# Kernel tuning notes

Measured on AMD Instinct MI355X. Metric: run time of the kernel, lower is better.

Reference implementation:

```python
import math
import jax, jax.numpy as jnp
import numpy as np

B, T, C, H = 4, 2048, 1024, 1024

def setup_inputs() -> dict:
    key = jax.random.key(0)
    kx, kk, kq, kv = jax.random.split(key, 4)
    s = 1.0 / math.sqrt(C)
    return {
        "x": jax.random.normal(kx, (B, T, C), dtype=jnp.float32),
        # torch Linear weight is [out, in]; store transposed [in, out] for x @ W
        "Wk": jax.random.uniform(kk, (C, H), dtype=jnp.float32, minval=-s, maxval=s),
        "Wq": jax.random.uniform(kq, (C, H), dtype=jnp.float32, minval=-s, maxval=s),
        "Wv": jax.random.uniform(kv, (C, H), dtype=jnp.float32, minval=-s, maxval=s),
    }

def reference(x, Wk, Wq, Wv):
    K = x @ Wk  # [B,T,H]
    Q = x @ Wq
    V = x @ Wv
    scale = 1.0 / math.sqrt(K.shape[-1])
    wei = jnp.einsum('bth,bsh->bts', Q, K) * scale  # [B,T,T]
    t = x.shape[1]
    causal = jnp.tril(jnp.ones((t, t), dtype=bool))
    wei = jnp.where(causal, wei, -jnp.inf)
    wei = jax.nn.softmax(wei, axis=-1)
    wei = jax.nn.relu(wei)  # no-op mathematically but kept for fidelity
    return jnp.einsum('bts,bsh->bth', wei, V)
```

## Files before the change

### kernel.cpp

```cpp
#include <hip/hip_runtime.h>

typedef _Float16 f16;
typedef _Float16 f16x8 __attribute__((ext_vector_type(8)));
typedef float    f32x4 __attribute__((ext_vector_type(4)));

#define AS3 __attribute__((address_space(3)))
#define AS1 __attribute__((address_space(1)))

static __device__ __forceinline__ void gld_lds16(const f16* g, f16* l) {
    __builtin_amdgcn_global_load_lds((const AS1 void*)g, (AS3 void*)l, 16, 0, 0);
}

static __device__ __forceinline__ unsigned pack_f16(float a, float b) {
    union { f16 h[2]; unsigned u; } p;
    p.h[0] = (f16)a; p.h[1] = (f16)b;
    return p.u;
}

__global__ void cvt_fused(const float* __restrict__ x, f16* __restrict__ xh,
                          const float* __restrict__ Wq, const float* __restrict__ Wk,
                          const float* __restrict__ Wv, f16* __restrict__ Wt) {
    __shared__ float tile[32][33];
    const int bid = blockIdx.x;
    if (bid < 4096) {
        int i = bid * 256 + threadIdx.x;
        const f32x4* xv = (const f32x4*)x;
        f32x4 a = xv[2 * i], b = xv[2 * i + 1];
        f16x8 h;
        h[0] = (f16)a[0]; h[1] = (f16)a[1]; h[2] = (f16)a[2]; h[3] = (f16)a[3];
        h[4] = (f16)b[0]; h[5] = (f16)b[1]; h[6] = (f16)b[2]; h[7] = (f16)b[3];
        ((f16x8*)xh)[i] = h;
    } else {
        int b2 = bid - 4096;
        int bx = b2 & 31, by = (b2 >> 5) & 31, bz = b2 >> 10;
        const float* W = bz == 0 ? Wq : (bz == 1 ? Wk : Wv);
        int tx = threadIdx.x & 31, ty = threadIdx.x >> 5;
        int n0 = bx * 32, k0 = by * 32;
#pragma unroll
        for (int r = 0; r < 4; ++r)
            tile[ty + r * 8][tx] = W[(size_t)(k0 + ty + r * 8) * 1024 + n0 + tx];
        __syncthreads();
        f16* o = Wt + (size_t)bz * 1024 * 1024;
#pragma unroll
        for (int r = 0; r < 4; ++r)
            o[(size_t)(n0 + ty + r * 8) * 1024 + k0 + tx] = (f16)tile[tx][ty + r * 8];
    }
}

template <int MODE>
__global__ __launch_bounds__(256, 4)
void gemm128(const f16* __restrict__ A, int lda, long aStride,
             const f16* __restrict__ B, int ldb, long bStride,
             void* __restrict__ Cout, int ldc, long cStride,
             int ktiles, float scale,
             const f16* __restrict__ A2, const f16* __restrict__ B2,
             void* __restrict__ C2) {
    int bm, bn, bz = blockIdx.z;
    int m0, n0;
    const f16 *Ab, *Bb;
    char* Cb;

    if (MODE == 0) {
        bn = blockIdx.x; bm = blockIdx.y;
        n0 = bn * 128;
        if (bm < 64) {
            m0 = bm * 128;
            Ab = A; Bb = B; Cb = (char*)Cout;
        } else {
            int t = bm - 64;
            int bb = t >> 3;
            m0 = (t & 7) * 128;
            Ab = A2;
            Bb = B2 + (long)bb * 2048 * 1024;
            Cb = (char*)C2 + (long)bb * 1024 * 2048 * sizeof(f16);
        }
    } else if (MODE == 1) {
        int i = blockIdx.x;
        float ff = sqrtf(8.f * (float)i + 1.f);
        bm = (int)((ff - 1.f) * 0.5f);
        while ((bm + 1) * (bm + 2) / 2 <= i) ++bm;
        while (bm * (bm + 1) / 2 > i) --bm;
        bn = i - bm * (bm + 1) / 2;
        m0 = bm * 128; n0 = bn * 128;
        Ab = A + (long)bz * aStride;
        Bb = B + (long)bz * bStride;
        Cb = (char*)Cout + (long)bz * cStride * sizeof(f16);
    } else {
        bn = blockIdx.x; bm = gridDim.y - 1 - blockIdx.y;
        int lim = 4 * (bm + 1); if (lim < ktiles) ktiles = lim;
        m0 = bm * 128; n0 = bn * 128;
        Ab = A + (long)bz * aStride;
        Bb = B + (long)bz * bStride;
        Cb = (char*)Cout + (long)bz * cStride * sizeof(float);
    }

    __shared__ f16 lds[2 * 8192];

    const int tid = threadIdx.x;
    const int wave = tid >> 6, lane = tid & 63;
    const int q = lane >> 4, rr = lane & 15;
    const int wm = (wave >> 1) * 64, wn = (wave & 1) * 64;

    const int kcs = (((tid & 3) - (lane >> 4)) & 3) * 8;
    const f16* pA = Ab + (long)(m0 + (tid >> 2)) * lda + kcs;
    const f16* pB = Bb + (long)(n0 + (tid >> 2)) * ldb + kcs;

    auto stage = [&](int kt, int buf) {
        const int k0 = kt * 32;
        f16* lA = lds + buf * 8192 + wave * 512;
        f16* lB = lds + buf * 8192 + 4096 + wave * 512;
#pragma unroll
        for (int it = 0; it < 2; ++it) {
            gld_lds16(pA + (long)it * 64 * lda + k0, lA + it * 2048);
            gld_lds16(pB + (long)it * 64 * ldb + k0, lB + it * 2048);
        }
    };

    const int slotf = ((q + (rr >> 2)) & 3) * 8;

    f32x4 acc[4][4] = {};
    f32x4 accs[4] = {};
    f16x8 onef;
    const bool sumwave = (MODE == 2) && (wn == 0);
    if (MODE == 2) {
#pragma unroll
        for (int t = 0; t < 8; ++t) onef[t] = (f16)1.0f;
    }

    stage(0, 0);
    __syncthreads();

    for (int kt = 0; kt < ktiles; ++kt) {
        const int cur = kt & 1;
        if (kt + 1 < ktiles) stage(kt + 1, 1 - cur);
        const f16* bufA = lds + cur * 8192;
        const f16* bufB = bufA + 4096;
        f16x8 af[4], bf[4];
#pragma unroll
        for (int i = 0; i < 4; ++i)
            af[i] = *(const f16x8*)&bufA[(wm + i * 16 + rr) * 32 + slotf];
#pragma unroll
        for (int j = 0; j < 4; ++j)
            bf[j] = *(const f16x8*)&bufB[(wn + j * 16 + rr) * 32 + slotf];
#pragma unroll
        for (int i = 0; i < 4; ++i) {
#pragma unroll
            for (int j = 0; j < 4; ++j)
                acc[i][j] = __builtin_amdgcn_mfma_f32_16x16x32_f16(af[i], bf[j], acc[i][j], 0, 0, 0);
            if (sumwave)
                accs[i] = __builtin_amdgcn_mfma_f32_16x16x32_f16(af[i], onef, accs[i], 0, 0, 0);
        }
        __syncthreads();
    }

    float invr[4][4];
    if (MODE == 2) {
        float* rs = (float*)lds;
        if (sumwave && rr == 0) {
#pragma unroll
            for (int i = 0; i < 4; ++i)
#pragma unroll
                for (int r2 = 0; r2 < 4; ++r2)
                    rs[wm + i * 16 + q * 4 + r2] = accs[i][r2];
        }
        __syncthreads();
#pragma unroll
        for (int i = 0; i < 4; ++i)
#pragma unroll
            for (int r2 = 0; r2 < 4; ++r2)
                invr[i][r2] = 1.0f / rs[wm + i * 16 + q * 4 + r2];
    }

#pragma unroll
    for (int i = 0; i < 4; ++i) {
#pragma unroll
        for (int r2 = 0; r2 < 4; ++r2) {
            const int row = wm + i * 16 + q * 4 + r2;
#pragma unroll
            for (int j = 0; j < 4; ++j) {
                const int col = wn + j * 16 + rr;
                float v = acc[i][j][r2] * scale;
                long idx = (long)(m0 + row) * ldc + n0 + col;
                if (MODE == 1) {
                    v = __expf(v);
                    if (n0 + col > m0 + row) v = 0.f;
                    float vo = __shfl_xor(v, 1, 64);
                    if ((rr & 1) == 0)
                        *(unsigned*)((f16*)Cb + idx) = pack_f16(v, vo);
                } else if (MODE == 0) {
                    float vo = __shfl_xor(v, 1, 64);
                    if ((rr & 1) == 0)
                        *(unsigned*)((f16*)Cb + idx) = pack_f16(v, vo);
                } else {
                    v *= invr[i][r2];
                    float vo = __shfl_xor(v, 1, 64);
                    if ((rr & 1) == 0)
                        *(float2*)((float*)Cb + idx) = make_float2(v, vo);
                }
            }
        }
    }
}

extern "C" void kernel_launch(void* const* d_in, const int* in_sizes, int n_in,
                              void* d_out, int out_size, void* d_ws, size_t ws_size,
                              hipStream_t stream) {
    (void)in_sizes; (void)n_in; (void)out_size; (void)ws_size;
    const float* x  = (const float*)d_in[0];
    const float* Wk = (const float*)d_in[1];
    const float* Wq = (const float*)d_in[2];
    const float* Wv = (const float*)d_in[3];
    float* out = (float*)d_out;

    const long MB = 1l << 20;
    char* ws = (char*)d_ws;
    f16*   qk   = (f16*)(ws);
    f16*   Vt   = (f16*)(ws + 32 * MB);
    f16*   P    = (f16*)(ws + 48 * MB);
    f16*   xh   = (f16*)(ws + 81 * MB);
    f16*   Wt   = (f16*)(ws + 97 * MB);

    cvt_fused<<<7168, 256, 0, stream>>>(x, xh, Wq, Wk, Wv, Wt);

    gemm128<0><<<dim3(16, 96, 1), 256, 0, stream>>>(xh, 1024, 0, Wt, 1024, 0,
                                                    qk, 2048, 0, 32, 1.0f,
                                                    Wt + 2l * 1024 * 1024, xh, Vt);
    gemm128<1><<<dim3(136, 1, 4), 256, 0, stream>>>(qk, 2048, 2048l * 2048,
                                                    qk + 1024, 2048, 2048l * 2048,
                                                    P, 2048, 2048l * 2048, 32, 0.03125f,
                                                    nullptr, nullptr, nullptr);
    gemm128<2><<<dim3(8, 16, 4), 256, 0, stream>>>(P, 2048, 2048l * 2048,
                                                   Vt, 2048, 1024l * 2048,
                                                   out, 1024, 2048l * 1024, 64, 1.0f,
                                                   nullptr, nullptr, nullptr);
}
```

Measured before the change: 255.9 us.

## Replace QKV projection GEMM with 256x256-tile, 512-thread pipelined kernel

After: 249.0 us. -2.7%, faster.

```diff
diff --git a/kernel.cpp b/kernel.cpp
--- a/kernel.cpp
+++ b/kernel.cpp
@@ -47,6 +47,114 @@
     }
 }
 
+#define KT 16
+
+__global__ __launch_bounds__(512, 2)
+void gemm256(const f16* __restrict__ Axh, const f16* __restrict__ Bw, f16* __restrict__ Cqk,
+             const f16* __restrict__ Awv, const f16* __restrict__ Bxh, f16* __restrict__ CVt) {
+    const int orig = blockIdx.x;
+    const int wg = (orig & 7) * 48 + (orig >> 3);
+    int m0, n0; const f16 *Ab, *Bb; f16* Cb;
+    if (wg < 256) {
+        m0 = (wg >> 3) * 256; n0 = (wg & 7) * 256;
+        Ab = Axh; Bb = Bw; Cb = Cqk;
+    } else {
+        int t = wg - 256, bb = t >> 5, r = t & 31;
+        m0 = (r >> 3) * 256; n0 = (r & 7) * 256;
+        Ab = Awv; Bb = Bxh + (long)bb * 2048 * 1024; Cb = CVt + (long)bb * 1024 * 2048;
+    }
+    const int lda = 1024, ldb = 1024, ldc = 2048;
+
+    __shared__ f16 lds[2 * 32768];
+
+    const int tid = threadIdx.x;
+    const int wave = tid >> 6, lane = tid & 63;
+    const int q = lane >> 4, rr = lane & 15;
+    const int wr = wave >> 2, wc = wave & 3;
+
+    const int kcs = (((lane & 7) - (lane >> 3)) & 7) * 8;
+    const f16* pA = Ab + (long)(m0 + (tid >> 3)) * lda + kcs;
+    const f16* pB = Bb + (long)(n0 + (tid >> 3)) * ldb + kcs;
+    const int ldsw = wave * 512;
+
+    auto stageA = [&](int kt, int h, int buf) {
+        f16* dst = lds + buf * 32768 + h * 8192 + ldsw;
+        const f16* src = pA + (long)(h * 128) * lda + kt * 64;
+        gld_lds16(src, dst);
+        gld_lds16(src + (long)64 * lda, dst + 4096);
+    };
+    auto stageB = [&](int kt, int h, int buf) {
+        f16* dst = lds + buf * 32768 + 16384 + h * 8192 + ldsw;
+        const f16* src = pB + (long)(h * 128) * ldb + kt * 64;
+        gld_lds16(src, dst);
+        gld_lds16(src + (long)64 * ldb, dst + 4096);
+    };
+
+    f32x4 acc[8][4] = {};
+
+    stageA(0, 0, 0); stageA(0, 1, 0); stageB(0, 0, 0); stageB(0, 1, 0);
+    stageB(1 < KT ? 1 : KT - 1, 0, 1); stageB(1 < KT ? 1 : KT - 1, 1, 1);
+    asm volatile("s_waitcnt vmcnt(4)" ::: "memory");
+    __builtin_amdgcn_s_barrier();
+
+    for (int u = 0; u < KT; ++u) {
+        const int cur = u & 1;
+        const f16* bA = lds + cur * 32768 + wr * 8192;
+        const f16* bB = lds + cur * 32768 + 16384 + (wc >> 1) * 8192;
+        const int brow = (wc & 1) * 64;
+        const int ua = u + 1 < KT ? u + 1 : KT - 1;
+        const int ub = u + 2 < KT ? u + 2 : KT - 1;
+        const int bufA_ = (u + 1) & 1, bufB_ = cur;
+        f16x8 bf[4][2];
+#pragma unroll
+        for (int p = 0; p < 4; ++p) {
+            f16x8 a[2][2];
+            if (p == 0) {
+#pragma unroll
+                for (int j = 0; j < 4; ++j)
+#pragma unroll
+                    for (int ks = 0; ks < 2; ++ks)
+                        bf[j][ks] = *(const f16x8*)&bB[(brow + j * 16 + rr) * 64 + ((ks * 4 + q + rr) & 7) * 8];
+            }
+#pragma unroll
+            for (int fi = 0; fi < 2; ++fi)
+#pragma unroll
+                for (int ks = 0; ks < 2; ++ks)
+                    a[fi][ks] = *(const f16x8*)&bA[((p * 2 + fi) * 16 + rr) * 64 + ((ks * 4 + q + rr) & 7) * 8];
+            if      (p == 0) stageA(ua, 0, bufA_);
+            else if (p == 1) stageA(ua, 1, bufA_);
+            else if (p == 2) stageB(ub, 0, bufB_);
+            else             stageB(ub, 1, bufB_);
+            __builtin_amdgcn_s_barrier();
+            asm volatile("s_waitcnt lgkmcnt(0)" ::: "memory");
+            __builtin_amdgcn_sched_barrier(0);
+            __builtin_amdgcn_s_setprio(1);
+#pragma unroll
+            for (int ks = 0; ks < 2; ++ks)
+#pragma unroll
+                for (int fi = 0; fi < 2; ++fi)
+#pragma unroll
+                    for (int j = 0; j < 4; ++j)
+                        acc[p * 2 + fi][j] = __builtin_amdgcn_mfma_f32_16x16x32_f16(
+                            a[fi][ks], bf[j][ks], acc[p * 2 + fi][j], 0, 0, 0);
+            __builtin_amdgcn_s_setprio(0);
+            if (p == 3) asm volatile("s_waitcnt vmcnt(4)" ::: "memory");
+            __builtin_amdgcn_s_barrier();
+        }
+    }
+    asm volatile("s_waitcnt vmcnt(0)" ::: "memory");
+
+#pragma unroll
+    for (int i = 0; i < 8; ++i)
+#pragma unroll
+        for (int r2 = 0; r2 < 4; ++r2) {
+            const long row = m0 + wr * 128 + i * 16 + q * 4 + r2;
+#pragma unroll
+            for (int j = 0; j < 4; ++j)
+                Cb[row * ldc + n0 + wc * 64 + j * 16 + rr] = (f16)acc[i][j][r2];
+        }
+}
+
 template <int MODE>
 __global__ __launch_bounds__(256, 4)
 void gemm128(const f16* __restrict__ A, int lda, long aStride,
@@ -60,21 +168,7 @@
     const f16 *Ab, *Bb;
     char* Cb;
 
-    if (MODE == 0) {
-        bn = blockIdx.x; bm = blockIdx.y;
-        n0 = bn * 128;
-        if (bm < 64) {
-            m0 = bm * 128;
-            Ab = A; Bb = B; Cb = (char*)Cout;
-        } else {
-            int t = bm - 64;
-            int bb = t >> 3;
-            m0 = (t & 7) * 128;
-            Ab = A2;
-            Bb = B2 + (long)bb * 2048 * 1024;
-            Cb = (char*)C2 + (long)bb * 1024 * 2048 * sizeof(f16);
-        }
-    } else if (MODE == 1) {
+    if (MODE == 1) {
         int i = blockIdx.x;
         float ff = sqrtf(8.f * (float)i + 1.f);
         bm = (int)((ff - 1.f) * 0.5f);
@@ -187,10 +281,6 @@
                     float vo = __shfl_xor(v, 1, 64);
                     if ((rr & 1) == 0)
                         *(unsigned*)((f16*)Cb + idx) = pack_f16(v, vo);
-                } else if (MODE == 0) {
-                    float vo = __shfl_xor(v, 1, 64);
-                    if ((rr & 1) == 0)
-                        *(unsigned*)((f16*)Cb + idx) = pack_f16(v, vo);
                 } else {
                     v *= invr[i][r2];
                     float vo = __shfl_xor(v, 1, 64);
@@ -222,9 +312,8 @@
 
     cvt_fused<<<7168, 256, 0, stream>>>(x, xh, Wq, Wk, Wv, Wt);
 
-    gemm128<0><<<dim3(16, 96, 1), 256, 0, stream>>>(xh, 1024, 0, Wt, 1024, 0,
-                                                    qk, 2048, 0, 32, 1.0f,
-                                                    Wt + 2l * 1024 * 1024, xh, Vt);
+    gemm256<<<dim3(384), 512, 0, stream>>>(xh, Wt, qk,
+                                           Wt + 2l * 1024 * 1024, xh, Vt);
     gemm128<1><<<dim3(136, 1, 4), 256, 0, stream>>>(qk, 2048, 2048l * 2048,
                                                     qk + 1024, 2048, 2048l * 2048,
                                                     P, 2048, 2048l * 2048, 32, 0.03125f,
```
